# Kernel optimization log

Hardware: AMD Instinct MI355X
Metric: run time of the kernel (lower is better)

Reference implementation:

```python
import jax, jax.numpy as jnp
import numpy as np

EPS = 1e-5

def lrelu(x):
    return jnp.where(x >= 0, x, 0.1 * x)

def bn_eval(x, g, b, m, v):
    # eval-mode BatchNorm over the last (channel) axis
    return (x - m) * (g * jax.lax.rsqrt(v + EPS)) + b

def setup_inputs():
    key = jax.random.key(0)
    ks = jax.random.split(key, 12)
    Nq, K, Cin, Fc, Co = 20000, 32, 3, 64, 64
    q_points = jax.random.normal(ks[0], (Nq, Cin), jnp.float32)
    s_points = jax.random.normal(ks[1], (Nq, Cin), jnp.float32)
    feat = jax.random.normal(ks[2], (Nq, Fc), jnp.float32)
    # valid indices 0..Nq (Nq == shadow/pad row appended in forward)
    neighb_inds = jax.random.randint(ks[3], (Nq, K), 0, Nq + 1)
    def w(k, shape, fan_in):
        return jax.random.normal(k, shape, jnp.float32) / np.float32(np.sqrt(fan_in))
    W_pos2 = w(ks[4], (Fc, Cin), Cin)          # convpos2: Conv2d(Cin, Fc, 1)
    W_attn = w(ks[5], (Co * Cin, Fc), Fc)      # convattn: Conv2d(Fc, Co*Cin, 1)
    W_res = w(ks[6], (Co, Fc), Fc)             # residual 1x1 conv
    def bn(k, c):
        k1, k2, k3, k4 = jax.random.split(k, 4)
        return (jax.random.normal(k1, (c,), jnp.float32) * 0.1 + 1.0,
                jax.random.normal(k2, (c,), jnp.float32) * 0.1,
                jax.random.normal(k3, (c,), jnp.float32) * 0.1,
                jax.random.uniform(k4, (c,), jnp.float32) * 0.5 + 0.5)
    bq = bn(ks[7], Fc); bp = bn(ks[8], Cin); b1 = bn(ks[9], Co); br = bn(ks[10], Co)
    return dict(q_points=q_points, s_points=s_points, neighb_inds=neighb_inds, feat=feat,
                W_pos2=W_pos2, W_attn=W_attn, W_res=W_res,
                bnq_g=bq[0], bnq_b=bq[1], bnq_m=bq[2], bnq_v=bq[3],
                bnp_g=bp[0], bnp_b=bp[1], bnp_m=bp[2], bnp_v=bp[3],
                bn1_g=b1[0], bn1_b=b1[1], bn1_m=b1[2], bn1_v=b1[3],
                bnr_g=br[0], bnr_b=br[1], bnr_m=br[2], bnr_v=br[3])

def reference(q_points, s_points, neighb_inds, feat, W_pos2, W_attn, W_res,
              bnq_g, bnq_b, bnq_m, bnq_v, bnp_g, bnp_b, bnp_m, bnp_v,
              bn1_g, bn1_b, bn1_m, bn1_v, bnr_g, bnr_b, bnr_m, bnr_v):
    Nq, Cin = q_points.shape
    Fc = feat.shape[1]
    Co = W_res.shape[0]
    K = neighb_inds.shape[1]
    # append shadow (zero) row for out-of-range neighbor indices
    s_pad = jnp.concatenate([s_points, jnp.zeros((1, Cin), s_points.dtype)], 0)
    f_pad = jnp.concatenate([feat, jnp.zeros((1, Fc), feat.dtype)], 0)
    xg = s_pad[neighb_inds]                      # [Nq,K,Cin] EFR_P gather
    yg = f_pad[neighb_inds]                      # [Nq,K,Fc]  EFR_F gather
    x_v = xg - q_points[:, None, :]              # [Nq,K,Cin] values
    x_q = lrelu(bn_eval(feat, bnq_g, bnq_b, bnq_m, bnq_v))          # [Nq,Fc]
    pos0 = lrelu(bn_eval(s_points, bnp_g, bnp_b, bnp_m, bnp_v))     # [Nq,Cin]
    pos = (pos0[:, None, :] - x_v) @ W_pos2.T                       # [Nq,K,Fc]
    attn = x_q[:, None, :] - yg + pos                               # [Nq,K,Fc]
    attn = jax.nn.softmax(attn / jnp.sqrt(jnp.float32(Fc)), axis=1) # softmax over K
    attn = (attn @ W_attn.T).reshape(Nq, K, Co, Cin)                # [Nq,K,Co,Cin]
    y_e = jnp.einsum('nkoi,nki->nko', attn, x_v)                    # [Nq,K,Co]
    y_e = lrelu(bn_eval(y_e, bn1_g, bn1_b, bn1_m, bn1_v))
    res = bn_eval(yg @ W_res.T, bnr_g, bnr_b, bnr_m, bnr_v)         # [Nq,K,Co]
    y_e = lrelu(y_e + res)
    return y_e.max(axis=1)                                          # [Nq,Co]
```

## Files before the change

kernel.cpp:

```cpp
#include <hip/hip_runtime.h>
#include <math.h>

#define KNB 32
#define FC 64
#define CO 64
#define EPS 1e-5f
#define NBLOCKS 1024
#define CL 0.180336880095853f

typedef __attribute__((ext_vector_type(8))) short short8;
typedef __attribute__((ext_vector_type(4))) float floatx4;

#if __has_builtin(__builtin_amdgcn_exp2f)
#define EXP2F(x) __builtin_amdgcn_exp2f(x)
#else
#define EXP2F(x) exp2f(x)
#endif
#if __has_builtin(__builtin_amdgcn_rcpf)
#define RCPF(x) __builtin_amdgcn_rcpf(x)
#else
#define RCPF(x) (1.f / (x))
#endif

__device__ __forceinline__ unsigned int pkbf(float a, float b) {
    unsigned int ua = (__float_as_uint(a) + 0x8000u) >> 16;
    unsigned int ub = (__float_as_uint(b) + 0x8000u) & 0xFFFF0000u;
    return ua | ub;
}
__device__ __forceinline__ short f2bf(float x) {
    return (short)((__float_as_uint(x) + 0x8000u) >> 16);
}
__device__ __forceinline__ float lrelu(float x) { return fmaxf(x, 0.1f * x); }

__global__ __launch_bounds__(256, 4) void GCT_61272003445298_kernel(
    const float* __restrict__ q_points,
    const float* __restrict__ s_points,
    const int*   __restrict__ neighb,
    const float* __restrict__ feat,
    const float* __restrict__ W_pos2,
    const float* __restrict__ W_attn,
    const float* __restrict__ W_res,
    const float* __restrict__ bnq_g, const float* __restrict__ bnq_b,
    const float* __restrict__ bnq_m, const float* __restrict__ bnq_v,
    const float* __restrict__ bnp_g, const float* __restrict__ bnp_b,
    const float* __restrict__ bnp_m, const float* __restrict__ bnp_v,
    const float* __restrict__ bn1_g, const float* __restrict__ bn1_b,
    const float* __restrict__ bn1_m, const float* __restrict__ bn1_v,
    const float* __restrict__ bnr_g, const float* __restrict__ bnr_b,
    const float* __restrict__ bnr_m, const float* __restrict__ bnr_v,
    float* __restrict__ out, int Nq)
{
    const int t = threadIdx.x;
    const int wv = t >> 6;
    const int lane = t & 63;
    const int cc = lane & 15, quad = lane >> 4;
    const int o = wv * 16 + cc;

    const int qB  = t >> 7;
    const int kg  = lane >> 3;
    const int fqB = (((t >> 6) & 1) << 3) + (lane & 7);

    __shared__ __align__(16) short sA1[64 * 72];
    __shared__ __align__(16) short sA2[64 * 72];
    __shared__ float sXv[64][4];
    __shared__ __align__(16) float sWp2[192];
    __shared__ __align__(16) float sQs[64], sQb[64];

    if (t < 192) sWp2[t] = CL * W_pos2[t];
    if (t < 64) {
        float sc = bnq_g[t] * rsqrtf(bnq_v[t] + EPS);
        sQs[t] = sc; sQb[t] = bnq_b[t] - bnq_m[t] * sc;
    }
    float ps[3], pb[3];
    #pragma unroll
    for (int i = 0; i < 3; ++i) {
        float sc = bnp_g[i] * rsqrtf(bnp_v[i] + EPS);
        ps[i] = sc; pb[i] = bnp_b[i] - bnp_m[i] * sc;
    }
    const float e1s = bn1_g[o] * rsqrtf(bn1_v[o] + EPS);
    const float e1b = bn1_b[o] - bn1_m[o] * e1s;
    const float ers = bnr_g[o] * rsqrtf(bnr_v[o] + EPS);
    const float erb = bnr_b[o] - bnr_m[o] * ers;

    short8 bW[4][2];
    #pragma unroll
    for (int ty = 0; ty < 4; ++ty) {
        const float* wrow = (ty < 3) ? (W_attn + (long)(o * 3 + ty) * FC)
                                     : (W_res  + (long)o * FC);
        #pragma unroll
        for (int ks = 0; ks < 2; ++ks) {
            int k0 = ks * 32 + quad * 8;
            float4 w0 = *(const float4*)(wrow + k0);
            float4 w1 = *(const float4*)(wrow + k0 + 4);
            short8 b;
            b[0] = f2bf(w0.x); b[1] = f2bf(w0.y); b[2] = f2bf(w0.z); b[3] = f2bf(w0.w);
            b[4] = f2bf(w1.x); b[5] = f2bf(w1.y); b[6] = f2bf(w1.z); b[7] = f2bf(w1.w);
            bW[ty][ks] = b;
        }
    }
    __syncthreads();

    float wp[12];
    *(float4*)&wp[0] = *(const float4*)&sWp2[fqB * 12];
    *(float4*)&wp[4] = *(const float4*)&sWp2[fqB * 12 + 4];
    *(float4*)&wp[8] = *(const float4*)&sWp2[fqB * 12 + 8];

    const float4* __restrict__ feat4 = (const float4*)feat;
    const bool xvWriter = ((t & 0x47) == 0);

    const int npair = (Nq + 1) >> 1;
    for (int p = blockIdx.x; p < npair; p += NBLOCKS) {
        const long n0 = 2L * p;
        long n1 = n0 + 1;
        const bool has1 = (n1 < Nq);
        if (!has1) n1 = n0;
        const long nn = qB ? n1 : n0;

        float nqp0 = -q_points[nn * 3 + 0];
        float nqp1 = -q_points[nn * 3 + 1];
        float nqp2 = -q_points[nn * 3 + 2];
        float p0 = lrelu(fmaf(s_points[nn * 3 + 0], ps[0], pb[0]));
        float p1 = lrelu(fmaf(s_points[nn * 3 + 1], ps[1], pb[1]));
        float p2 = lrelu(fmaf(s_points[nn * 3 + 2], ps[2], pb[2]));
        int4 idx4 = *(const int4*)(neighb + nn * KNB + kg * 4);

        float4 qs4 = *(const float4*)&sQs[fqB * 4];
        float4 qb4 = *(const float4*)&sQb[fqB * 4];
        float4 fx  = feat4[(int)(nn * 16) + fqB];
        float4 xqc;
        {
            float x0 = lrelu(fmaf(fx.x, qs4.x, qb4.x));
            float x1 = lrelu(fmaf(fx.y, qs4.y, qb4.y));
            float x2 = lrelu(fmaf(fx.z, qs4.z, qb4.z));
            float x3 = lrelu(fmaf(fx.w, qs4.w, qb4.w));
            xqc.x = fmaf(p0, wp[0], fmaf(p1, wp[1],  fmaf(p2, wp[2],  CL * x0)));
            xqc.y = fmaf(p0, wp[3], fmaf(p1, wp[4],  fmaf(p2, wp[5],  CL * x1)));
            xqc.z = fmaf(p0, wp[6], fmaf(p1, wp[7],  fmaf(p2, wp[8],  CL * x2)));
            xqc.w = fmaf(p0, wp[9], fmaf(p1, wp[10], fmaf(p2, wp[11], CL * x3)));
        }

        float ev[4][4];
        float s0 = 0.f, s1 = 0.f, s2 = 0.f, s3 = 0.f;
        #pragma unroll
        for (int j = 0; j < 4; ++j) {
            const int idx = ((const int*)&idx4)[j];
            const int row = qB * 32 + kg * 4 + j;
            const float sel = (idx < Nq) ? 1.f : 0.f;
            const int idc = (idx < Nq) ? idx : 0;
            float4 y = feat4[idc * 16 + fqB];
            y.x *= sel; y.y *= sel; y.z *= sel; y.w *= sel;
            uint2 pk; pk.x = pkbf(y.x, y.y); pk.y = pkbf(y.z, y.w);
            *(uint2*)(sA2 + row * 72 + fqB * 4) = pk;
            float xv0 = fmaf(s_points[idc * 3 + 0], sel, nqp0);
            float xv1 = fmaf(s_points[idc * 3 + 1], sel, nqp1);
            float xv2 = fmaf(s_points[idc * 3 + 2], sel, nqp2);
            if (xvWriter) {
                sXv[row][0] = xv0; sXv[row][1] = xv1; sXv[row][2] = xv2;
                sXv[row][3] = 0.f;
            }
            float l0 = fmaf(y.x, -CL, xqc.x);
            l0 = fmaf(-xv0, wp[0], l0); l0 = fmaf(-xv1, wp[1], l0); l0 = fmaf(-xv2, wp[2], l0);
            float l1 = fmaf(y.y, -CL, xqc.y);
            l1 = fmaf(-xv0, wp[3], l1); l1 = fmaf(-xv1, wp[4], l1); l1 = fmaf(-xv2, wp[5], l1);
            float l2 = fmaf(y.z, -CL, xqc.z);
            l2 = fmaf(-xv0, wp[6], l2); l2 = fmaf(-xv1, wp[7], l2); l2 = fmaf(-xv2, wp[8], l2);
            float l3 = fmaf(y.w, -CL, xqc.w);
            l3 = fmaf(-xv0, wp[9], l3); l3 = fmaf(-xv1, wp[10], l3); l3 = fmaf(-xv2, wp[11], l3);
            ev[j][0] = EXP2F(l0); ev[j][1] = EXP2F(l1);
            ev[j][2] = EXP2F(l2); ev[j][3] = EXP2F(l3);
            s0 += ev[j][0]; s1 += ev[j][1]; s2 += ev[j][2]; s3 += ev[j][3];
        }
        s0 += __shfl_xor(s0, 8); s0 += __shfl_xor(s0, 16); s0 += __shfl_xor(s0, 32);
        s1 += __shfl_xor(s1, 8); s1 += __shfl_xor(s1, 16); s1 += __shfl_xor(s1, 32);
        s2 += __shfl_xor(s2, 8); s2 += __shfl_xor(s2, 16); s2 += __shfl_xor(s2, 32);
        s3 += __shfl_xor(s3, 8); s3 += __shfl_xor(s3, 16); s3 += __shfl_xor(s3, 32);
        const float i0 = RCPF(s0), i1 = RCPF(s1), i2 = RCPF(s2), i3 = RCPF(s3);
        #pragma unroll
        for (int j = 0; j < 4; ++j) {
            const int row = qB * 32 + kg * 4 + j;
            uint2 pw;
            pw.x = pkbf(ev[j][0] * i0, ev[j][1] * i1);
            pw.y = pkbf(ev[j][2] * i2, ev[j][3] * i3);
            *(uint2*)(sA1 + row * 72 + fqB * 4) = pw;
        }
        __syncthreads();

        float m0 = -1e30f, m1 = -1e30f;
        #pragma unroll
        for (int mt = 0; mt < 4; ++mt) {
            floatx4 acc[4];
            #pragma unroll
            for (int ty = 0; ty < 4; ++ty) acc[ty] = (floatx4){0.f, 0.f, 0.f, 0.f};
            int r0 = mt * 16 + cc;
            #pragma unroll
            for (int ks = 0; ks < 2; ++ks) {
                int kof = ks * 32 + quad * 8;
                short8 a1 = *(const short8*)(sA1 + r0 * 72 + kof);
                short8 a2 = *(const short8*)(sA2 + r0 * 72 + kof);
                acc[0] = __builtin_amdgcn_mfma_f32_16x16x32_bf16(a1, bW[0][ks], acc[0], 0, 0, 0);
                acc[1] = __builtin_amdgcn_mfma_f32_16x16x32_bf16(a1, bW[1][ks], acc[1], 0, 0, 0);
                acc[2] = __builtin_amdgcn_mfma_f32_16x16x32_bf16(a1, bW[2][ks], acc[2], 0, 0, 0);
                acc[3] = __builtin_amdgcn_mfma_f32_16x16x32_bf16(a2, bW[3][ks], acc[3], 0, 0, 0);
            }
            #pragma unroll
            for (int reg = 0; reg < 4; ++reg) {
                int r = mt * 16 + quad * 4 + reg;
                float4 xv = *(const float4*)&sXv[r][0];
                float y = acc[0][reg] * xv.x + acc[1][reg] * xv.y + acc[2][reg] * xv.z;
                float ybn = lrelu(y * e1s + e1b);
                float rbn = acc[3][reg] * ers + erb;
                float v = lrelu(ybn + rbn);
                if (mt < 2) m0 = fmaxf(m0, v); else m1 = fmaxf(m1, v);
            }
        }
        m0 = fmaxf(m0, __shfl_xor(m0, 16));
        m0 = fmaxf(m0, __shfl_xor(m0, 32));
        m1 = fmaxf(m1, __shfl_xor(m1, 16));
        m1 = fmaxf(m1, __shfl_xor(m1, 32));
        if (lane < 16) {
            out[n0 * CO + o] = m0;
            if (has1) out[n1 * CO + o] = m1;
        }
        __syncthreads();
    }
}

extern "C" void kernel_launch(void* const* d_in, const int* in_sizes, int n_in,
                              void* d_out, int out_size, void* d_ws, size_t ws_size,
                              hipStream_t stream) {
    const float* q_points = (const float*)d_in[0];
    const float* s_points = (const float*)d_in[1];
    const int*   neighb   = (const int*)  d_in[2];
    const float* feat     = (const float*)d_in[3];
    const float* W_pos2   = (const float*)d_in[4];
    const float* W_attn   = (const float*)d_in[5];
    const float* W_res    = (const float*)d_in[6];
    const float* bnq_g = (const float*)d_in[7];
    const float* bnq_b = (const float*)d_in[8];
    const float* bnq_m = (const float*)d_in[9];
    const float* bnq_v = (const float*)d_in[10];
    const float* bnp_g = (const float*)d_in[11];
    const float* bnp_b = (const float*)d_in[12];
    const float* bnp_m = (const float*)d_in[13];
    const float* bnp_v = (const float*)d_in[14];
    const float* bn1_g = (const float*)d_in[15];
    const float* bn1_b = (const float*)d_in[16];
    const float* bn1_m = (const float*)d_in[17];
    const float* bn1_v = (const float*)d_in[18];
    const float* bnr_g = (const float*)d_in[19];
    const float* bnr_b = (const float*)d_in[20];
    const float* bnr_m = (const float*)d_in[21];
    const float* bnr_v = (const float*)d_in[22];
    float* out = (float*)d_out;

    int Nq = in_sizes[0] / 3;

    hipLaunchKernelGGL(GCT_61272003445298_kernel,
                       dim3(NBLOCKS), dim3(256), 0, stream,
                       q_points, s_points, neighb, feat, W_pos2, W_attn, W_res,
                       bnq_g, bnq_b, bnq_m, bnq_v,
                       bnp_g, bnp_b, bnp_m, bnp_v,
                       bn1_g, bn1_b, bn1_m, bn1_v,
                       bnr_g, bnr_b, bnr_m, bnr_v,
                       out, Nq);
}
```

Before: 161.4 us.

## Split block into producer and consumer wavefronts with double-buffered LDS

Turns the kernel into a warp-specialized pipeline. Two wavefronts gather neighbors and compute the softmax into one of two LDS buffers for the next point pair. Meanwhile two MFMA wavefronts each cover 32 output channels and consume the current buffer. Invalid neighbor rows now read from a zeroed workspace page set by a memset, so the select multiplies go away. The grid drops to 768 blocks with launch bounds for 3 blocks per unit. The trade-offs are more registers per consumer thread, double the LDS use, and an extra memset launch that may count toward the timed region.

Result: slower. 192.4 us (+19.2%).

```diff
diff --git a/kernel.cpp b/kernel.cpp
--- a/kernel.cpp
+++ b/kernel.cpp
@@ -5,7 +5,7 @@
 #define FC 64
 #define CO 64
 #define EPS 1e-5f
-#define NBLOCKS 1024
+#define NBLOCKS 768
 #define CL 0.180336880095853f
 
 typedef __attribute__((ext_vector_type(8))) short short8;
@@ -32,7 +32,7 @@
 }
 __device__ __forceinline__ float lrelu(float x) { return fmaxf(x, 0.1f * x); }
 
-__global__ __launch_bounds__(256, 4) void GCT_61272003445298_kernel(
+__global__ __launch_bounds__(256, 3) void GCT_61272003445298_kernel(
     const float* __restrict__ q_points,
     const float* __restrict__ s_points,
     const int*   __restrict__ neighb,
@@ -48,21 +48,17 @@
     const float* __restrict__ bn1_m, const float* __restrict__ bn1_v,
     const float* __restrict__ bnr_g, const float* __restrict__ bnr_b,
     const float* __restrict__ bnr_m, const float* __restrict__ bnr_v,
+    const float* __restrict__ zp,
     float* __restrict__ out, int Nq)
 {
     const int t = threadIdx.x;
     const int wv = t >> 6;
     const int lane = t & 63;
-    const int cc = lane & 15, quad = lane >> 4;
-    const int o = wv * 16 + cc;
-
-    const int qB  = t >> 7;
-    const int kg  = lane >> 3;
-    const int fqB = (((t >> 6) & 1) << 3) + (lane & 7);
-
-    __shared__ __align__(16) short sA1[64 * 72];
-    __shared__ __align__(16) short sA2[64 * 72];
-    __shared__ float sXv[64][4];
+    const int bid = blockIdx.x;
+
+    __shared__ __align__(16) short sA1[2][64 * 72];
+    __shared__ __align__(16) short sA2[2][64 * 72];
+    __shared__ __align__(16) float sXv[2][64][4];
     __shared__ __align__(16) float sWp2[192];
     __shared__ __align__(16) float sQs[64], sQb[64];
 
@@ -71,155 +67,196 @@
         float sc = bnq_g[t] * rsqrtf(bnq_v[t] + EPS);
         sQs[t] = sc; sQb[t] = bnq_b[t] - bnq_m[t] * sc;
     }
-    float ps[3], pb[3];
-    #pragma unroll
-    for (int i = 0; i < 3; ++i) {
-        float sc = bnp_g[i] * rsqrtf(bnp_v[i] + EPS);
-        ps[i] = sc; pb[i] = bnp_b[i] - bnp_m[i] * sc;
+    const float ps0 = bnp_g[0] * rsqrtf(bnp_v[0] + EPS);
+    const float ps1 = bnp_g[1] * rsqrtf(bnp_v[1] + EPS);
+    const float ps2 = bnp_g[2] * rsqrtf(bnp_v[2] + EPS);
+    const float pb0 = bnp_b[0] - bnp_m[0] * ps0;
+    const float pb1 = bnp_b[1] - bnp_m[1] * ps1;
+    const float pb2 = bnp_b[2] - bnp_m[2] * ps2;
+    __syncthreads();
+
+    const bool producer = (wv < 2);
+    const int npair = (Nq + 1) >> 1;
+    const int niter = (npair - bid + NBLOCKS - 1) / NBLOCKS;
+
+    const int qB = __builtin_amdgcn_readfirstlane(wv & 1);
+    const int kg = lane >> 3;
+    const int fi = lane & 7;
+    float wp[24];
+    const int cc = lane & 15, quad = lane >> 4;
+    short8 bW[2][4][2];
+    float e1s[2], e1b[2], ers[2], erb[2];
+
+    if (producer) {
+        #pragma unroll
+        for (int v = 0; v < 6; ++v)
+            *(float4*)&wp[v * 4] = *(const float4*)&sWp2[fi * 24 + v * 4];
+    } else {
+        const int cwv = wv - 2;
+        #pragma unroll
+        for (int g = 0; g < 2; ++g) {
+            const int o = cwv * 32 + g * 16 + cc;
+            float s1v = bn1_g[o] * rsqrtf(bn1_v[o] + EPS);
+            e1s[g] = s1v; e1b[g] = bn1_b[o] - bn1_m[o] * s1v;
+            float srv = bnr_g[o] * rsqrtf(bnr_v[o] + EPS);
+            ers[g] = srv; erb[g] = bnr_b[o] - bnr_m[o] * srv;
+            #pragma unroll
+            for (int ty = 0; ty < 4; ++ty) {
+                const float* wrow = (ty < 3) ? (W_attn + (long)(o * 3 + ty) * FC)
+                                             : (W_res  + (long)o * FC);
+                #pragma unroll
+                for (int ks = 0; ks < 2; ++ks) {
+                    int k0 = ks * 32 + quad * 8;
+                    float4 w0 = *(const float4*)(wrow + k0);
+                    float4 w1 = *(const float4*)(wrow + k0 + 4);
+                    short8 bb;
+                    bb[0] = f2bf(w0.x); bb[1] = f2bf(w0.y); bb[2] = f2bf(w0.z); bb[3] = f2bf(w0.w);
+                    bb[4] = f2bf(w1.x); bb[5] = f2bf(w1.y); bb[6] = f2bf(w1.z); bb[7] = f2bf(w1.w);
+                    bW[g][ty][ks] = bb;
+                }
+            }
+        }
     }
-    const float e1s = bn1_g[o] * rsqrtf(bn1_v[o] + EPS);
-    const float e1b = bn1_b[o] - bn1_m[o] * e1s;
-    const float ers = bnr_g[o] * rsqrtf(bnr_v[o] + EPS);
-    const float erb = bnr_b[o] - bnr_m[o] * ers;
-
-    short8 bW[4][2];
-    #pragma unroll
-    for (int ty = 0; ty < 4; ++ty) {
-        const float* wrow = (ty < 3) ? (W_attn + (long)(o * 3 + ty) * FC)
-                                     : (W_res  + (long)o * FC);
-        #pragma unroll
-        for (int ks = 0; ks < 2; ++ks) {
-            int k0 = ks * 32 + quad * 8;
-            float4 w0 = *(const float4*)(wrow + k0);
-            float4 w1 = *(const float4*)(wrow + k0 + 4);
-            short8 b;
-            b[0] = f2bf(w0.x); b[1] = f2bf(w0.y); b[2] = f2bf(w0.z); b[3] = f2bf(w0.w);
-            b[4] = f2bf(w1.x); b[5] = f2bf(w1.y); b[6] = f2bf(w1.z); b[7] = f2bf(w1.w);
-            bW[ty][ks] = b;
-        }
-    }
-    __syncthreads();
-
-    float wp[12];
-    *(float4*)&wp[0] = *(const float4*)&sWp2[fqB * 12];
-    *(float4*)&wp[4] = *(const float4*)&sWp2[fqB * 12 + 4];
-    *(float4*)&wp[8] = *(const float4*)&sWp2[fqB * 12 + 8];
-
-    const float4* __restrict__ feat4 = (const float4*)feat;
-    const bool xvWriter = ((t & 0x47) == 0);
-
-    const int npair = (Nq + 1) >> 1;
-    for (int p = blockIdx.x; p < npair; p += NBLOCKS) {
-        const long n0 = 2L * p;
-        long n1 = n0 + 1;
-        const bool has1 = (n1 < Nq);
-        if (!has1) n1 = n0;
-        const long nn = qB ? n1 : n0;
-
-        float nqp0 = -q_points[nn * 3 + 0];
-        float nqp1 = -q_points[nn * 3 + 1];
-        float nqp2 = -q_points[nn * 3 + 2];
-        float p0 = lrelu(fmaf(s_points[nn * 3 + 0], ps[0], pb[0]));
-        float p1 = lrelu(fmaf(s_points[nn * 3 + 1], ps[1], pb[1]));
-        float p2 = lrelu(fmaf(s_points[nn * 3 + 2], ps[2], pb[2]));
-        int4 idx4 = *(const int4*)(neighb + nn * KNB + kg * 4);
-
-        float4 qs4 = *(const float4*)&sQs[fqB * 4];
-        float4 qb4 = *(const float4*)&sQb[fqB * 4];
-        float4 fx  = feat4[(int)(nn * 16) + fqB];
-        float4 xqc;
+
+    auto produce = [&](int pr, int b) {
+        int nn = 2 * pr + qB;
+        if (nn >= Nq) nn = 2 * pr;
+        const float* qp  = q_points + (long)nn * 3;
+        const float q0 = qp[0], q1 = qp[1], q2 = qp[2];
+        const float* spn = s_points + (long)nn * 3;
+        const float pp0 = lrelu(fmaf(spn[0], ps0, pb0));
+        const float pp1 = lrelu(fmaf(spn[1], ps1, pb1));
+        const float pp2 = lrelu(fmaf(spn[2], ps2, pb2));
+        const int4 idx4 = *(const int4*)(neighb + (long)nn * KNB + kg * 4);
+
+        float xqc[8];
         {
-            float x0 = lrelu(fmaf(fx.x, qs4.x, qb4.x));
-            float x1 = lrelu(fmaf(fx.y, qs4.y, qb4.y));
-            float x2 = lrelu(fmaf(fx.z, qs4.z, qb4.z));
-            float x3 = lrelu(fmaf(fx.w, qs4.w, qb4.w));
-            xqc.x = fmaf(p0, wp[0], fmaf(p1, wp[1],  fmaf(p2, wp[2],  CL * x0)));
-            xqc.y = fmaf(p0, wp[3], fmaf(p1, wp[4],  fmaf(p2, wp[5],  CL * x1)));
-            xqc.z = fmaf(p0, wp[6], fmaf(p1, wp[7],  fmaf(p2, wp[8],  CL * x2)));
-            xqc.w = fmaf(p0, wp[9], fmaf(p1, wp[10], fmaf(p2, wp[11], CL * x3)));
-        }
-
-        float ev[4][4];
-        float s0 = 0.f, s1 = 0.f, s2 = 0.f, s3 = 0.f;
+            const float4 fxa = *(const float4*)(feat + (long)nn * FC + fi * 8);
+            const float4 fxb = *(const float4*)(feat + (long)nn * FC + fi * 8 + 4);
+            const float4 qsa = *(const float4*)&sQs[fi * 8];
+            const float4 qsb = *(const float4*)&sQs[fi * 8 + 4];
+            const float4 qba = *(const float4*)&sQb[fi * 8];
+            const float4 qbb = *(const float4*)&sQb[fi * 8 + 4];
+            const float fx[8] = {fxa.x, fxa.y, fxa.z, fxa.w, fxb.x, fxb.y, fxb.z, fxb.w};
+            const float qs[8] = {qsa.x, qsa.y, qsa.z, qsa.w, qsb.x, qsb.y, qsb.z, qsb.w};
+            const float qb[8] = {qba.x, qba.y, qba.z, qba.w, qbb.x, qbb.y, qbb.z, qbb.w};
+            #pragma unroll
+            for (int c = 0; c < 8; ++c) {
+                float xq = lrelu(fmaf(fx[c], qs[c], qb[c]));
+                xqc[c] = fmaf(pp0, wp[c*3], fmaf(pp1, wp[c*3+1], fmaf(pp2, wp[c*3+2], CL * xq)));
+            }
+        }
+
+        short* a1b = &sA1[b][(qB * 32 + kg * 4) * 72 + fi * 8];
+        short* a2b = &sA2[b][(qB * 32 + kg * 4) * 72 + fi * 8];
+        float ev[4][8];
+        float sm[8] = {0.f, 0.f, 0.f, 0.f, 0.f, 0.f, 0.f, 0.f};
         #pragma unroll
         for (int j = 0; j < 4; ++j) {
             const int idx = ((const int*)&idx4)[j];
-            const int row = qB * 32 + kg * 4 + j;
-            const float sel = (idx < Nq) ? 1.f : 0.f;
-            const int idc = (idx < Nq) ? idx : 0;
-            float4 y = feat4[idc * 16 + fqB];
-            y.x *= sel; y.y *= sel; y.z *= sel; y.w *= sel;
-            uint2 pk; pk.x = pkbf(y.x, y.y); pk.y = pkbf(y.z, y.w);
-            *(uint2*)(sA2 + row * 72 + fqB * 4) = pk;
-            float xv0 = fmaf(s_points[idc * 3 + 0], sel, nqp0);
-            float xv1 = fmaf(s_points[idc * 3 + 1], sel, nqp1);
-            float xv2 = fmaf(s_points[idc * 3 + 2], sel, nqp2);
-            if (xvWriter) {
-                sXv[row][0] = xv0; sXv[row][1] = xv1; sXv[row][2] = xv2;
-                sXv[row][3] = 0.f;
-            }
-            float l0 = fmaf(y.x, -CL, xqc.x);
-            l0 = fmaf(-xv0, wp[0], l0); l0 = fmaf(-xv1, wp[1], l0); l0 = fmaf(-xv2, wp[2], l0);
-            float l1 = fmaf(y.y, -CL, xqc.y);
-            l1 = fmaf(-xv0, wp[3], l1); l1 = fmaf(-xv1, wp[4], l1); l1 = fmaf(-xv2, wp[5], l1);
-            float l2 = fmaf(y.z, -CL, xqc.z);
-            l2 = fmaf(-xv0, wp[6], l2); l2 = fmaf(-xv1, wp[7], l2); l2 = fmaf(-xv2, wp[8], l2);
-            float l3 = fmaf(y.w, -CL, xqc.w);
-            l3 = fmaf(-xv0, wp[9], l3); l3 = fmaf(-xv1, wp[10], l3); l3 = fmaf(-xv2, wp[11], l3);
-            ev[j][0] = EXP2F(l0); ev[j][1] = EXP2F(l1);
-            ev[j][2] = EXP2F(l2); ev[j][3] = EXP2F(l3);
-            s0 += ev[j][0]; s1 += ev[j][1]; s2 += ev[j][2]; s3 += ev[j][3];
-        }
-        s0 += __shfl_xor(s0, 8); s0 += __shfl_xor(s0, 16); s0 += __shfl_xor(s0, 32);
-        s1 += __shfl_xor(s1, 8); s1 += __shfl_xor(s1, 16); s1 += __shfl_xor(s1, 32);
-        s2 += __shfl_xor(s2, 8); s2 += __shfl_xor(s2, 16); s2 += __shfl_xor(s2, 32);
-        s3 += __shfl_xor(s3, 8); s3 += __shfl_xor(s3, 16); s3 += __shfl_xor(s3, 32);
-        const float i0 = RCPF(s0), i1 = RCPF(s1), i2 = RCPF(s2), i3 = RCPF(s3);
+            const bool valid = (idx < Nq);
+            const float* fb = valid ? (feat + (long)idx * FC) : zp;
+            const float* sb = valid ? (s_points + (long)idx * 3) : zp;
+            const float4 ya = *(const float4*)(fb + fi * 8);
+            const float4 yb = *(const float4*)(fb + fi * 8 + 4);
+            const float xv0 = sb[0] - q0;
+            const float xv1 = sb[1] - q1;
+            const float xv2 = sb[2] - q2;
+            if (fi == 0) {
+                float4 xvv = {xv0, xv1, xv2, 0.f};
+                *(float4*)&sXv[b][qB * 32 + kg * 4 + j][0] = xvv;
+            }
+            uint4 pk;
+            pk.x = pkbf(ya.x, ya.y); pk.y = pkbf(ya.z, ya.w);
+            pk.z = pkbf(yb.x, yb.y); pk.w = pkbf(yb.z, yb.w);
+            *(uint4*)(a2b + j * 72) = pk;
+            const float y[8] = {ya.x, ya.y, ya.z, ya.w, yb.x, yb.y, yb.z, yb.w};
+            #pragma unroll
+            for (int c = 0; c < 8; ++c) {
+                float l = fmaf(y[c], -CL, xqc[c]);
+                l = fmaf(-xv0, wp[c*3], l);
+                l = fmaf(-xv1, wp[c*3+1], l);
+                l = fmaf(-xv2, wp[c*3+2], l);
+                float e = EXP2F(l);
+                ev[j][c] = e;
+                sm[c] += e;
+            }
+        }
+        #pragma unroll
+        for (int c = 0; c < 8; ++c) {
+            float s = sm[c];
+            s += __shfl_xor(s, 8);
+            s += __shfl_xor(s, 16);
+            s += __shfl_xor(s, 32);
+            sm[c] = RCPF(s);
+        }
         #pragma unroll
         for (int j = 0; j < 4; ++j) {
-            const int row = qB * 32 + kg * 4 + j;
-            uint2 pw;
-            pw.x = pkbf(ev[j][0] * i0, ev[j][1] * i1);
-            pw.y = pkbf(ev[j][2] * i2, ev[j][3] * i3);
-            *(uint2*)(sA1 + row * 72 + fqB * 4) = pw;
-        }
-        __syncthreads();
-
-        float m0 = -1e30f, m1 = -1e30f;
-        #pragma unroll
-        for (int mt = 0; mt < 4; ++mt) {
-            floatx4 acc[4];
+            uint4 pw;
+            pw.x = pkbf(ev[j][0] * sm[0], ev[j][1] * sm[1]);
+            pw.y = pkbf(ev[j][2] * sm[2], ev[j][3] * sm[3]);
+            pw.z = pkbf(ev[j][4] * sm[4], ev[j][5] * sm[5]);
+            pw.w = pkbf(ev[j][6] * sm[6], ev[j][7] * sm[7]);
+            *(uint4*)(a1b + j * 72) = pw;
+        }
+    };
+
+    auto consume = [&](int pc, int b) {
+        const long n0 = 2L * pc;
+        const long n1 = n0 + 1;
+        const bool has1 = (n1 < Nq);
+        const int cwv = wv - 2;
+        #pragma unroll
+        for (int g = 0; g < 2; ++g) {
+            float m0 = -1e30f, m1 = -1e30f;
             #pragma unroll
-            for (int ty = 0; ty < 4; ++ty) acc[ty] = (floatx4){0.f, 0.f, 0.f, 0.f};
-            int r0 = mt * 16 + cc;
-            #pragma unroll
-            for (int ks = 0; ks < 2; ++ks) {
-                int kof = ks * 32 + quad * 8;
-                short8 a1 = *(const short8*)(sA1 + r0 * 72 + kof);
-                short8 a2 = *(const short8*)(sA2 + r0 * 72 + kof);
-                acc[0] = __builtin_amdgcn_mfma_f32_16x16x32_bf16(a1, bW[0][ks], acc[0], 0, 0, 0);
-                acc[1] = __builtin_amdgcn_mfma_f32_16x16x32_bf16(a1, bW[1][ks], acc[1], 0, 0, 0);
-                acc[2] = __builtin_amdgcn_mfma_f32_16x16x32_bf16(a1, bW[2][ks], acc[2], 0, 0, 0);
-                acc[3] = __builtin_amdgcn_mfma_f32_16x16x32_bf16(a2, bW[3][ks], acc[3], 0, 0, 0);
-            }
-            #pragma unroll
-            for (int reg = 0; reg < 4; ++reg) {
-                int r = mt * 16 + quad * 4 + reg;
-                float4 xv = *(const float4*)&sXv[r][0];
-                float y = acc[0][reg] * xv.x + acc[1][reg] * xv.y + acc[2][reg] * xv.z;
-                float ybn = lrelu(y * e1s + e1b);
-                float rbn = acc[3][reg] * ers + erb;
-                float v = lrelu(ybn + rbn);
-                if (mt < 2) m0 = fmaxf(m0, v); else m1 = fmaxf(m1, v);
-            }
-        }
-        m0 = fmaxf(m0, __shfl_xor(m0, 16));
-        m0 = fmaxf(m0, __shfl_xor(m0, 32));
-        m1 = fmaxf(m1, __shfl_xor(m1, 16));
-        m1 = fmaxf(m1, __shfl_xor(m1, 32));
-        if (lane < 16) {
-            out[n0 * CO + o] = m0;
-            if (has1) out[n1 * CO + o] = m1;
+            for (int mt = 0; mt < 4; ++mt) {
+                floatx4 acc[4];
+                #pragma unroll
+                for (int ty = 0; ty < 4; ++ty) acc[ty] = (floatx4){0.f, 0.f, 0.f, 0.f};
+                const int r0 = mt * 16 + cc;
+                #pragma unroll
+                for (int ks = 0; ks < 2; ++ks) {
+                    const int kof = ks * 32 + quad * 8;
+                    short8 a1 = *(const short8*)&sA1[b][r0 * 72 + kof];
+                    short8 a2 = *(const short8*)&sA2[b][r0 * 72 + kof];
+                    acc[0] = __builtin_amdgcn_mfma_f32_16x16x32_bf16(a1, bW[g][0][ks], acc[0], 0, 0, 0);
+                    acc[1] = __builtin_amdgcn_mfma_f32_16x16x32_bf16(a1, bW[g][1][ks], acc[1], 0, 0, 0);
+                    acc[2] = __builtin_amdgcn_mfma_f32_16x16x32_bf16(a1, bW[g][2][ks], acc[2], 0, 0, 0);
+                    acc[3] = __builtin_amdgcn_mfma_f32_16x16x32_bf16(a2, bW[g][3][ks], acc[3], 0, 0, 0);
+                }
+                #pragma unroll
+                for (int reg = 0; reg < 4; ++reg) {
+                    const int r = mt * 16 + quad * 4 + reg;
+                    float4 xv = *(const float4*)&sXv[b][r][0];
+                    float y = acc[0][reg] * xv.x + acc[1][reg] * xv.y + acc[2][reg] * xv.z;
+                    float ybn = lrelu(fmaf(y, e1s[g], e1b[g]));
+                    float rbn = fmaf(acc[3][reg], ers[g], erb[g]);
+                    float v = lrelu(ybn + rbn);
+                    if (mt < 2) m0 = fmaxf(m0, v); else m1 = fmaxf(m1, v);
+                }
+            }
+            m0 = fmaxf(m0, __shfl_xor(m0, 16));
+            m0 = fmaxf(m0, __shfl_xor(m0, 32));
+            m1 = fmaxf(m1, __shfl_xor(m1, 16));
+            m1 = fmaxf(m1, __shfl_xor(m1, 32));
+            if (lane < 16) {
+                const int o = cwv * 32 + g * 16 + cc;
+                out[n0 * CO + o] = m0;
+                if (has1) out[n1 * CO + o] = m1;
+            }
+        }
+    };
+
+    if (producer) produce(bid, 0);
+    __syncthreads();
+    for (int i = 0; i < niter; ++i) {
+        const int buf = i & 1;
+        if (producer) {
+            const int pp = bid + (i + 1) * NBLOCKS;
+            if (pp < npair) produce(pp, buf ^ 1);
+        } else {
+            consume(bid + i * NBLOCKS, buf);
         }
         __syncthreads();
     }
@@ -255,6 +292,9 @@
 
     int Nq = in_sizes[0] / 3;
 
+    size_t zn = ws_size < 4096 ? ws_size : (size_t)4096;
+    hipMemsetAsync(d_ws, 0, zn, stream);
+
     hipLaunchKernelGGL(GCT_61272003445298_kernel,
                        dim3(NBLOCKS), dim3(256), 0, stream,
                        q_points, s_points, neighb, feat, W_pos2, W_attn, W_res,
@@ -262,5 +302,5 @@
                        bnp_g, bnp_b, bnp_m, bnp_v,
                        bn1_g, bn1_b, bn1_m, bn1_v,
                        bnr_g, bnr_b, bnr_m, bnr_v,
-                       out, Nq);
+                       (const float*)d_ws, out, Nq);
 }
```

## Double-buffer LDS tiles and prefetch next pair's gathers while running MFMA

Applied to the files above, without the earlier changes.

Restructures the persistent loop into a software pipeline. Shared A tiles and Xv are double-buffered, and the global gathers for the next query pair are issued before the MFMA consume stage of the current pair, so gather latency overlaps compute. It also folds the BN scales into the bf16 weights, moves the residual BN shift and final lrelu to after the max, and routes invalid indices to a zeroed workspace buffer instead of multiplying by a select mask. It drops occupancy (launch bounds 4 to 3, 1024 to 768 blocks) and raises register and LDS pressure, and it adds a memset launch. Applying lrelu(m+erb) after the max is exact because lrelu is monotonic.

New measurement: 172.6 us. 7.0% more time.

```diff
diff --git a/kernel.cpp b/kernel.cpp
--- a/kernel.cpp
+++ b/kernel.cpp
@@ -1,11 +1,12 @@
 #include <hip/hip_runtime.h>
+#include <hip/hip_bf16.h>
 #include <math.h>
 
 #define KNB 32
 #define FC 64
 #define CO 64
 #define EPS 1e-5f
-#define NBLOCKS 1024
+#define NBLOCKS 768
 #define CL 0.180336880095853f
 
 typedef __attribute__((ext_vector_type(8))) short short8;
@@ -22,17 +23,13 @@
 #define RCPF(x) (1.f / (x))
 #endif
 
-__device__ __forceinline__ unsigned int pkbf(float a, float b) {
-    unsigned int ua = (__float_as_uint(a) + 0x8000u) >> 16;
-    unsigned int ub = (__float_as_uint(b) + 0x8000u) & 0xFFFF0000u;
-    return ua | ub;
-}
-__device__ __forceinline__ short f2bf(float x) {
-    return (short)((__float_as_uint(x) + 0x8000u) >> 16);
+__device__ __forceinline__ unsigned pk2(float a, float b) {
+    __hip_bfloat162 h = __float22bfloat162_rn(float2{a, b});
+    unsigned u; __builtin_memcpy(&u, &h, 4); return u;
 }
 __device__ __forceinline__ float lrelu(float x) { return fmaxf(x, 0.1f * x); }
 
-__global__ __launch_bounds__(256, 4) void GCT_61272003445298_kernel(
+__global__ __launch_bounds__(256, 3) void GCT_61272003445298_kernel(
     const float* __restrict__ q_points,
     const float* __restrict__ s_points,
     const int*   __restrict__ neighb,
@@ -48,21 +45,22 @@
     const float* __restrict__ bn1_m, const float* __restrict__ bn1_v,
     const float* __restrict__ bnr_g, const float* __restrict__ bnr_b,
     const float* __restrict__ bnr_m, const float* __restrict__ bnr_v,
+    const float* __restrict__ zp,
     float* __restrict__ out, int Nq)
 {
     const int t = threadIdx.x;
     const int wv = t >> 6;
     const int lane = t & 63;
+    const int bid = blockIdx.x;
     const int cc = lane & 15, quad = lane >> 4;
     const int o = wv * 16 + cc;
-
     const int qB  = t >> 7;
     const int kg  = lane >> 3;
     const int fqB = (((t >> 6) & 1) << 3) + (lane & 7);
 
-    __shared__ __align__(16) short sA1[64 * 72];
-    __shared__ __align__(16) short sA2[64 * 72];
-    __shared__ float sXv[64][4];
+    __shared__ __align__(16) short sA1[2][64 * 72];
+    __shared__ __align__(16) short sA2[2][64 * 72];
+    __shared__ __align__(16) float sXv[2][64][4];
     __shared__ __align__(16) float sWp2[192];
     __shared__ __align__(16) float sQs[64], sQb[64];
 
@@ -71,12 +69,12 @@
         float sc = bnq_g[t] * rsqrtf(bnq_v[t] + EPS);
         sQs[t] = sc; sQb[t] = bnq_b[t] - bnq_m[t] * sc;
     }
-    float ps[3], pb[3];
-    #pragma unroll
-    for (int i = 0; i < 3; ++i) {
-        float sc = bnp_g[i] * rsqrtf(bnp_v[i] + EPS);
-        ps[i] = sc; pb[i] = bnp_b[i] - bnp_m[i] * sc;
-    }
+    const float ps0 = bnp_g[0] * rsqrtf(bnp_v[0] + EPS);
+    const float ps1 = bnp_g[1] * rsqrtf(bnp_v[1] + EPS);
+    const float ps2 = bnp_g[2] * rsqrtf(bnp_v[2] + EPS);
+    const float pb0 = bnp_b[0] - bnp_m[0] * ps0;
+    const float pb1 = bnp_b[1] - bnp_m[1] * ps1;
+    const float pb2 = bnp_b[2] - bnp_m[2] * ps2;
     const float e1s = bn1_g[o] * rsqrtf(bn1_v[o] + EPS);
     const float e1b = bn1_b[o] - bn1_m[o] * e1s;
     const float ers = bnr_g[o] * rsqrtf(bnr_v[o] + EPS);
@@ -87,15 +85,18 @@
     for (int ty = 0; ty < 4; ++ty) {
         const float* wrow = (ty < 3) ? (W_attn + (long)(o * 3 + ty) * FC)
                                      : (W_res  + (long)o * FC);
+        const float sc = (ty < 3) ? e1s : ers;
         #pragma unroll
         for (int ks = 0; ks < 2; ++ks) {
             int k0 = ks * 32 + quad * 8;
             float4 w0 = *(const float4*)(wrow + k0);
             float4 w1 = *(const float4*)(wrow + k0 + 4);
-            short8 b;
-            b[0] = f2bf(w0.x); b[1] = f2bf(w0.y); b[2] = f2bf(w0.z); b[3] = f2bf(w0.w);
-            b[4] = f2bf(w1.x); b[5] = f2bf(w1.y); b[6] = f2bf(w1.z); b[7] = f2bf(w1.w);
-            bW[ty][ks] = b;
+            uint4 pv;
+            pv.x = pk2(w0.x * sc, w0.y * sc);
+            pv.y = pk2(w0.z * sc, w0.w * sc);
+            pv.z = pk2(w1.x * sc, w1.y * sc);
+            pv.w = pk2(w1.z * sc, w1.w * sc);
+            __builtin_memcpy(&bW[ty][ks], &pv, 16);
         }
     }
     __syncthreads();
@@ -104,67 +105,75 @@
     *(float4*)&wp[0] = *(const float4*)&sWp2[fqB * 12];
     *(float4*)&wp[4] = *(const float4*)&sWp2[fqB * 12 + 4];
     *(float4*)&wp[8] = *(const float4*)&sWp2[fqB * 12 + 8];
-
-    const float4* __restrict__ feat4 = (const float4*)feat;
-    const bool xvWriter = ((t & 0x47) == 0);
+    const float4 qs4 = *(const float4*)&sQs[fqB * 4];
+    const float4 qb4 = *(const float4*)&sQb[fqB * 4];
 
     const int npair = (Nq + 1) >> 1;
-    for (int p = blockIdx.x; p < npair; p += NBLOCKS) {
-        const long n0 = 2L * p;
-        long n1 = n0 + 1;
-        const bool has1 = (n1 < Nq);
-        if (!has1) n1 = n0;
-        const long nn = qB ? n1 : n0;
-
-        float nqp0 = -q_points[nn * 3 + 0];
-        float nqp1 = -q_points[nn * 3 + 1];
-        float nqp2 = -q_points[nn * 3 + 2];
-        float p0 = lrelu(fmaf(s_points[nn * 3 + 0], ps[0], pb[0]));
-        float p1 = lrelu(fmaf(s_points[nn * 3 + 1], ps[1], pb[1]));
-        float p2 = lrelu(fmaf(s_points[nn * 3 + 2], ps[2], pb[2]));
-        int4 idx4 = *(const int4*)(neighb + nn * KNB + kg * 4);
-
-        float4 qs4 = *(const float4*)&sQs[fqB * 4];
-        float4 qb4 = *(const float4*)&sQb[fqB * 4];
-        float4 fx  = feat4[(int)(nn * 16) + fqB];
-        float4 xqc;
+    const int niter = (npair - bid + NBLOCKS - 1) / NBLOCKS;
+
+    int4  idxCur, idxNext;
+    float4 gF[4];
+    float  gS0[4], gS1[4], gS2[4];
+    float4 oF;
+    float  oQ0, oQ1, oQ2, oS0, oS1, oS2;
+
+    auto loadNb = [&](int pr) -> int4 {
+        return *(const int4*)(neighb + (long)(2 * pr + qB) * KNB + kg * 4);
+    };
+    auto issueGathers = [&](int pr, int4 idx4) {
+        const long nn = 2L * pr + qB;
+        oQ0 = q_points[nn * 3 + 0]; oQ1 = q_points[nn * 3 + 1]; oQ2 = q_points[nn * 3 + 2];
+        oS0 = s_points[nn * 3 + 0]; oS1 = s_points[nn * 3 + 1]; oS2 = s_points[nn * 3 + 2];
+        oF  = *(const float4*)(feat + nn * FC + fqB * 4);
+        #pragma unroll
+        for (int j = 0; j < 4; ++j) {
+            const int idx = ((const int*)&idx4)[j];
+            const bool valid = (idx < Nq);
+            const float* fb = valid ? (feat + (long)idx * FC) : zp;
+            const float* sb = valid ? (s_points + (long)idx * 3) : zp;
+            gF[j] = *(const float4*)(fb + fqB * 4);
+            gS0[j] = sb[0]; gS1[j] = sb[1]; gS2[j] = sb[2];
+        }
+    };
+    auto computeProduce = [&](int b) {
+        const float pp0 = lrelu(fmaf(oS0, ps0, pb0));
+        const float pp1 = lrelu(fmaf(oS1, ps1, pb1));
+        const float pp2 = lrelu(fmaf(oS2, ps2, pb2));
+        float xqc[4];
         {
-            float x0 = lrelu(fmaf(fx.x, qs4.x, qb4.x));
-            float x1 = lrelu(fmaf(fx.y, qs4.y, qb4.y));
-            float x2 = lrelu(fmaf(fx.z, qs4.z, qb4.z));
-            float x3 = lrelu(fmaf(fx.w, qs4.w, qb4.w));
-            xqc.x = fmaf(p0, wp[0], fmaf(p1, wp[1],  fmaf(p2, wp[2],  CL * x0)));
-            xqc.y = fmaf(p0, wp[3], fmaf(p1, wp[4],  fmaf(p2, wp[5],  CL * x1)));
-            xqc.z = fmaf(p0, wp[6], fmaf(p1, wp[7],  fmaf(p2, wp[8],  CL * x2)));
-            xqc.w = fmaf(p0, wp[9], fmaf(p1, wp[10], fmaf(p2, wp[11], CL * x3)));
-        }
-
+            const float fx[4] = {oF.x, oF.y, oF.z, oF.w};
+            const float qs[4] = {qs4.x, qs4.y, qs4.z, qs4.w};
+            const float qb[4] = {qb4.x, qb4.y, qb4.z, qb4.w};
+            #pragma unroll
+            for (int c = 0; c < 4; ++c) {
+                float xq = lrelu(fmaf(fx[c], qs[c], qb[c]));
+                xqc[c] = fmaf(pp0, wp[c*3], fmaf(pp1, wp[c*3+1],
+                              fmaf(pp2, wp[c*3+2], CL * xq)));
+            }
+        }
+        short* a1b = &sA1[b][(qB * 32 + kg * 4) * 72 + fqB * 4];
+        short* a2b = &sA2[b][(qB * 32 + kg * 4) * 72 + fqB * 4];
         float ev[4][4];
         float s0 = 0.f, s1 = 0.f, s2 = 0.f, s3 = 0.f;
         #pragma unroll
         for (int j = 0; j < 4; ++j) {
-            const int idx = ((const int*)&idx4)[j];
-            const int row = qB * 32 + kg * 4 + j;
-            const float sel = (idx < Nq) ? 1.f : 0.f;
-            const int idc = (idx < Nq) ? idx : 0;
-            float4 y = feat4[idc * 16 + fqB];
-            y.x *= sel; y.y *= sel; y.z *= sel; y.w *= sel;
-            uint2 pk; pk.x = pkbf(y.x, y.y); pk.y = pkbf(y.z, y.w);
-            *(uint2*)(sA2 + row * 72 + fqB * 4) = pk;
-            float xv0 = fmaf(s_points[idc * 3 + 0], sel, nqp0);
-            float xv1 = fmaf(s_points[idc * 3 + 1], sel, nqp1);
-            float xv2 = fmaf(s_points[idc * 3 + 2], sel, nqp2);
-            if (xvWriter) {
-                sXv[row][0] = xv0; sXv[row][1] = xv1; sXv[row][2] = xv2;
-                sXv[row][3] = 0.f;
-            }
-            float l0 = fmaf(y.x, -CL, xqc.x);
+            const float xv0 = gS0[j] - oQ0;
+            const float xv1 = gS1[j] - oQ1;
+            const float xv2 = gS2[j] - oQ2;
+            if (fqB == 0) {
+                float4 xvv = {xv0, xv1, xv2, 0.f};
+                *(float4*)&sXv[b][qB * 32 + kg * 4 + j][0] = xvv;
+            }
+            const float4 y = gF[j];
+            uint2 pk; pk.x = pk2(y.x, y.y); pk.y = pk2(y.z, y.w);
+            *(uint2*)(a2b + j * 72) = pk;
+            float l0 = fmaf(y.x, -CL, xqc[0]);
             l0 = fmaf(-xv0, wp[0], l0); l0 = fmaf(-xv1, wp[1], l0); l0 = fmaf(-xv2, wp[2], l0);
-            float l1 = fmaf(y.y, -CL, xqc.y);
+            float l1 = fmaf(y.y, -CL, xqc[1]);
             l1 = fmaf(-xv0, wp[3], l1); l1 = fmaf(-xv1, wp[4], l1); l1 = fmaf(-xv2, wp[5], l1);
-            float l2 = fmaf(y.z, -CL, xqc.z);
+            float l2 = fmaf(y.z, -CL, xqc[2]);
             l2 = fmaf(-xv0, wp[6], l2); l2 = fmaf(-xv1, wp[7], l2); l2 = fmaf(-xv2, wp[8], l2);
-            float l3 = fmaf(y.w, -CL, xqc.w);
+            float l3 = fmaf(y.w, -CL, xqc[3]);
             l3 = fmaf(-xv0, wp[9], l3); l3 = fmaf(-xv1, wp[10], l3); l3 = fmaf(-xv2, wp[11], l3);
             ev[j][0] = EXP2F(l0); ev[j][1] = EXP2F(l1);
             ev[j][2] = EXP2F(l2); ev[j][3] = EXP2F(l3);
@@ -177,26 +186,28 @@
         const float i0 = RCPF(s0), i1 = RCPF(s1), i2 = RCPF(s2), i3 = RCPF(s3);
         #pragma unroll
         for (int j = 0; j < 4; ++j) {
-            const int row = qB * 32 + kg * 4 + j;
             uint2 pw;
-            pw.x = pkbf(ev[j][0] * i0, ev[j][1] * i1);
-            pw.y = pkbf(ev[j][2] * i2, ev[j][3] * i3);
-            *(uint2*)(sA1 + row * 72 + fqB * 4) = pw;
-        }
-        __syncthreads();
-
+            pw.x = pk2(ev[j][0] * i0, ev[j][1] * i1);
+            pw.y = pk2(ev[j][2] * i2, ev[j][3] * i3);
+            *(uint2*)(a1b + j * 72) = pw;
+        }
+    };
+    auto consume = [&](int pc, int b) {
+        const long n0 = 2L * pc;
+        const long n1 = n0 + 1;
+        const bool has1 = (n1 < Nq);
         float m0 = -1e30f, m1 = -1e30f;
         #pragma unroll
         for (int mt = 0; mt < 4; ++mt) {
             floatx4 acc[4];
             #pragma unroll
             for (int ty = 0; ty < 4; ++ty) acc[ty] = (floatx4){0.f, 0.f, 0.f, 0.f};
-            int r0 = mt * 16 + cc;
+            const int r0 = mt * 16 + cc;
             #pragma unroll
             for (int ks = 0; ks < 2; ++ks) {
-                int kof = ks * 32 + quad * 8;
-                short8 a1 = *(const short8*)(sA1 + r0 * 72 + kof);
-                short8 a2 = *(const short8*)(sA2 + r0 * 72 + kof);
+                const int kof = ks * 32 + quad * 8;
+                short8 a1 = *(const short8*)&sA1[b][r0 * 72 + kof];
+                short8 a2 = *(const short8*)&sA2[b][r0 * 72 + kof];
                 acc[0] = __builtin_amdgcn_mfma_f32_16x16x32_bf16(a1, bW[0][ks], acc[0], 0, 0, 0);
                 acc[1] = __builtin_amdgcn_mfma_f32_16x16x32_bf16(a1, bW[1][ks], acc[1], 0, 0, 0);
                 acc[2] = __builtin_amdgcn_mfma_f32_16x16x32_bf16(a1, bW[2][ks], acc[2], 0, 0, 0);
@@ -204,12 +215,10 @@
             }
             #pragma unroll
             for (int reg = 0; reg < 4; ++reg) {
-                int r = mt * 16 + quad * 4 + reg;
-                float4 xv = *(const float4*)&sXv[r][0];
+                const int r = mt * 16 + quad * 4 + reg;
+                float4 xv = *(const float4*)&sXv[b][r][0];
                 float y = acc[0][reg] * xv.x + acc[1][reg] * xv.y + acc[2][reg] * xv.z;
-                float ybn = lrelu(y * e1s + e1b);
-                float rbn = acc[3][reg] * ers + erb;
-                float v = lrelu(ybn + rbn);
+                float v = lrelu(y + e1b) + acc[3][reg];
                 if (mt < 2) m0 = fmaxf(m0, v); else m1 = fmaxf(m1, v);
             }
         }
@@ -218,9 +227,26 @@
         m1 = fmaxf(m1, __shfl_xor(m1, 16));
         m1 = fmaxf(m1, __shfl_xor(m1, 32));
         if (lane < 16) {
-            out[n0 * CO + o] = m0;
-            if (has1) out[n1 * CO + o] = m1;
-        }
+            out[n0 * CO + o] = lrelu(m0 + erb);
+            if (has1) out[n1 * CO + o] = lrelu(m1 + erb);
+        }
+    };
+
+    idxCur = loadNb(bid);
+    if (bid + NBLOCKS < npair) idxNext = loadNb(bid + NBLOCKS);
+    issueGathers(bid, idxCur);
+    computeProduce(0);
+    __syncthreads();
+    for (int i = 0; i < niter; ++i) {
+        const int buf = i & 1;
+        const int pp1 = bid + (i + 1) * NBLOCKS;
+        const int pp2 = bid + (i + 2) * NBLOCKS;
+        if (pp1 < npair) {
+            issueGathers(pp1, idxNext);
+            if (pp2 < npair) idxNext = loadNb(pp2);
+        }
+        consume(bid + i * NBLOCKS, buf);
+        if (pp1 < npair) computeProduce(buf ^ 1);
         __syncthreads();
     }
 }
@@ -255,6 +281,9 @@
 
     int Nq = in_sizes[0] / 3;
 
+    size_t zn = ws_size < 4096 ? ws_size : (size_t)4096;
+    hipMemsetAsync(d_ws, 0, zn, stream);
+
     hipLaunchKernelGGL(GCT_61272003445298_kernel,
                        dim3(NBLOCKS), dim3(256), 0, stream,
                        q_points, s_points, neighb, feat, W_pos2, W_attn, W_res,
@@ -262,5 +291,5 @@
                        bnp_g, bnp_b, bnp_m, bnp_v,
                        bn1_g, bn1_b, bn1_m, bn1_v,
                        bnr_g, bnr_b, bnr_m, bnr_v,
-                       out, Nq);
+                       (const float*)d_ws, out, Nq);
 }
```
